# Kernel optimization log

Measured on AMD Instinct MI355X. Metric: run time of the kernel, lower is better.

The kernel has to match this reference:

```python
import jax, jax.numpy as jnp
import numpy as np

D_MODEL = 512
N_PAIRS = D_MODEL // 2
B, T = 8, 4096


def setup_inputs() -> dict:
    key = jax.random.key(0)
    ks = jax.random.split(key, 7)
    scale = 1.0 / np.sqrt(D_MODEL)
    return {
        "x_seq": jax.random.normal(ks[0], (B, T, D_MODEL), dtype=jnp.float32),
        "W_angle": jax.random.uniform(ks[1], (D_MODEL, N_PAIRS), jnp.float32, -scale, scale),
        "b_angle": jnp.zeros((N_PAIRS,), jnp.float32),
        "W_decay": jax.random.uniform(ks[2], (D_MODEL, 1), jnp.float32, -scale, scale),
        "b_decay": jnp.full((1,), 1.4, jnp.float32),
        "W_input": jax.random.uniform(ks[3], (D_MODEL, D_MODEL), jnp.float32, -scale, scale),
        "b_input": jax.random.uniform(ks[4], (D_MODEL,), jnp.float32, -scale, scale),
    }


def _givens_ssm(x_seq, W_angle, b_angle, W_decay, b_decay, W_input, b_input):
    Bb, Tt, D = x_seq.shape
    P = D // 2
    angles = jnp.einsum("btd,dp->btp", x_seq, W_angle) + b_angle          # [B,T,P]
    decays = jax.nn.sigmoid(jnp.einsum("btd,dk->btk", x_seq, W_decay) + b_decay)[..., 0]  # [B,T]
    inj = jnp.einsum("btd,de->bte", x_seq, W_input) + b_input              # [B,T,D]
    inj = inj.reshape(Bb, Tt, P, 2)

    # scan over time: h_t = decay_t * Rot(angles_t) h_{t-1} + inj_t, pairwise 2x2 rotations
    def step(h, inp):
        a, d, u = inp  # a:[B,P], d:[B], u:[B,P,2]
        c, s = jnp.cos(a), jnp.sin(a)
        he = c * h[..., 0] - s * h[..., 1]
        ho = s * h[..., 0] + c * h[..., 1]
        h_new = d[:, None, None] * jnp.stack([he, ho], axis=-1) + u
        return h_new, h_new

    h0 = jnp.zeros((Bb, P, 2), x_seq.dtype)
    xs = (jnp.swapaxes(angles, 0, 1), jnp.swapaxes(decays, 0, 1), jnp.swapaxes(inj, 0, 1))
    _, states = jax.lax.scan(step, h0, xs)  # [T,B,P,2]
    return jnp.swapaxes(states, 0, 1).reshape(Bb, Tt, D)


def reference(x_seq, W_angle, b_angle, W_decay, b_decay, W_input, b_input):
    return _givens_ssm(x_seq, W_angle, b_angle, W_decay, b_decay, W_input, b_input)
```

## Files before the change

### kernel.cpp

```cpp
#include <hip/hip_runtime.h>
#include <math.h>

typedef _Float16 half_t;
typedef __attribute__((ext_vector_type(8))) _Float16 half8;
typedef __attribute__((ext_vector_type(4))) _Float16 half4;
typedef __attribute__((ext_vector_type(2))) _Float16 half2v;
typedef __attribute__((ext_vector_type(4))) float floatx4;

#define BATCH   8
#define SEQ     4096
#define DM      512
#define NP      256
#define M_TOT   32768
#define NTOT    768
#define CHUNKS  256
#define CHUNK_LEN 16

__device__ __forceinline__ void async_load16(const void* g, void* l) {
    __builtin_amdgcn_global_load_lds((const __attribute__((address_space(1))) void*)g,
                                     (__attribute__((address_space(3))) void*)l,
                                     16, 0, 0);
}

__global__ __launch_bounds__(256) void decay_convert(const float* __restrict__ X,
                                                     const float* __restrict__ Wd,
                                                     const float* __restrict__ bd,
                                                     float* __restrict__ dec,
                                                     half_t* __restrict__ Xh) {
    const int wave = threadIdx.x >> 6;
    const int lane = threadIdx.x & 63;
    const int row0 = blockIdx.x * 8 + wave * 2;
    const float4* x0 = (const float4*)(X + (size_t)row0 * DM);
    const float4* x1 = x0 + 128;
    const float4* wd = (const float4*)Wd;
    float4 a0 = x0[2 * lane], a1 = x0[2 * lane + 1];
    float4 b0 = x1[2 * lane], b1 = x1[2 * lane + 1];
    float4 w0 = wd[2 * lane], w1 = wd[2 * lane + 1];
    float s0 = a0.x * w0.x + a0.y * w0.y + a0.z * w0.z + a0.w * w0.w
             + a1.x * w1.x + a1.y * w1.y + a1.z * w1.z + a1.w * w1.w;
    float s1 = b0.x * w0.x + b0.y * w0.y + b0.z * w0.z + b0.w * w0.w
             + b1.x * w1.x + b1.y * w1.y + b1.z * w1.z + b1.w * w1.w;
    half8 h0 = {(half_t)a0.x, (half_t)a0.y, (half_t)a0.z, (half_t)a0.w,
                (half_t)a1.x, (half_t)a1.y, (half_t)a1.z, (half_t)a1.w};
    half8 h1 = {(half_t)b0.x, (half_t)b0.y, (half_t)b0.z, (half_t)b0.w,
                (half_t)b1.x, (half_t)b1.y, (half_t)b1.z, (half_t)b1.w};
    *(half8*)(Xh + (size_t)row0 * DM + lane * 8) = h0;
    *(half8*)(Xh + (size_t)(row0 + 1) * DM + lane * 8) = h1;
#pragma unroll
    for (int off = 32; off > 0; off >>= 1) {
        s0 += __shfl_down(s0, off, 64);
        s1 += __shfl_down(s1, off, 64);
    }
    if (lane == 0) {
        dec[row0]     = 1.0f / (1.0f + __expf(-(s0 + bd[0])));
        dec[row0 + 1] = 1.0f / (1.0f + __expf(-(s1 + bd[0])));
    }
}

__global__ __launch_bounds__(256) void wcat_transpose(const float* __restrict__ Wi,
                                                      const float* __restrict__ Wa,
                                                      half_t* __restrict__ Wt) {
    const int idx = blockIdx.x * 256 + threadIdx.x;
    const int n = idx >> 9;
    const int k = idx & 511;
    float v = (n < DM) ? Wi[(size_t)k * DM + n] : Wa[(size_t)k * NP + (n - DM)];
    Wt[idx] = (half_t)v;
}

__global__ __launch_bounds__(256) void gemm_fused(const half_t* __restrict__ Xh,
                                                  const half_t* __restrict__ Wt,
                                                  const float* __restrict__ bi,
                                                  const float* __restrict__ ba,
                                                  half_t* __restrict__ inj,
                                                  half_t* __restrict__ angles) {
    __shared__ __align__(16) char As[8192];
    __shared__ __align__(16) char Bs[8192];

    const int bm   = blockIdx.x;
    const int bn   = blockIdx.y;
    const int tid  = threadIdx.x;
    const int wave = tid >> 6;
    const int lane = tid & 63;
    const int quad = lane >> 4;
    const int l16  = lane & 15;
    const int wrow = wave >> 1;
    const int wcol = wave & 1;

    floatx4 acc[4][4];
#pragma unroll
    for (int i = 0; i < 4; ++i)
#pragma unroll
        for (int j = 0; j < 4; ++j) acc[i][j] = (floatx4){0.f, 0.f, 0.f, 0.f};

    const int s0 = wave * 128 + lane;
    const int s1 = s0 + 64;
    const int r0 = s0 >> 2, kql0 = (s0 & 3) ^ ((r0 >> 1) & 3);
    const int r1 = s1 >> 2, kql1 = (s1 & 3) ^ ((r1 >> 1) & 3);
    const half_t* gA0 = Xh + (size_t)(bm * 128 + r0) * DM + kql0 * 8;
    const half_t* gA1 = Xh + (size_t)(bm * 128 + r1) * DM + kql1 * 8;
    const half_t* gB0 = Wt + (size_t)(bn * 128 + r0) * DM + kql0 * 8;
    const half_t* gB1 = Wt + (size_t)(bn * 128 + r1) * DM + kql1 * 8;
    char* lA0 = As + wave * 2048;
    char* lA1 = As + wave * 2048 + 1024;
    char* lB0 = Bs + wave * 2048;
    char* lB1 = Bs + wave * 2048 + 1024;

    for (int k0 = 0; k0 < DM; k0 += 32) {
        async_load16(gA0 + k0, lA0);
        async_load16(gA1 + k0, lA1);
        async_load16(gB0 + k0, lB0);
        async_load16(gB1 + k0, lB1);
        __syncthreads();

        half8 af[4], bf[4];
#pragma unroll
        for (int mt = 0; mt < 4; ++mt) {
            const int r = wrow * 64 + mt * 16 + l16;
            af[mt] = *(const half8*)(As + r * 64 + ((quad ^ ((r >> 1) & 3)) << 4));
        }
#pragma unroll
        for (int nt = 0; nt < 4; ++nt) {
            const int r = wcol * 64 + nt * 16 + l16;
            bf[nt] = *(const half8*)(Bs + r * 64 + ((quad ^ ((r >> 1) & 3)) << 4));
        }
#pragma unroll
        for (int mt = 0; mt < 4; ++mt)
#pragma unroll
            for (int nt = 0; nt < 4; ++nt)
                acc[mt][nt] = __builtin_amdgcn_mfma_f32_16x16x32_f16(af[mt], bf[nt],
                                                                     acc[mt][nt], 0, 0, 0);
        __syncthreads();
    }

    const int colbase = bn * 128 + wcol * 64;
#pragma unroll
    for (int nt = 0; nt < 4; ++nt) {
        const int col = colbase + nt * 16 + l16;
        const bool is_inj = col < DM;
        const float bias = is_inj ? bi[col] : ba[col - DM];
#pragma unroll
        for (int mt = 0; mt < 4; ++mt) {
            const int rowb = bm * 128 + wrow * 64 + mt * 16 + quad * 4;
#pragma unroll
            for (int r = 0; r < 4; ++r) {
                const float v = acc[mt][nt][r] + bias;
                const int row = rowb + r;
                if (is_inj) inj[(size_t)row * DM + col] = (half_t)v;
                else        angles[(size_t)row * NP + (col - DM)] = (half_t)v;
            }
        }
    }
}

__global__ __launch_bounds__(256) void scan_sum1(const half_t* __restrict__ angles,
                                                 const float* __restrict__ decays,
                                                 const half_t* __restrict__ inj,
                                                 float* __restrict__ thetaC,
                                                 float4* __restrict__ hend,
                                                 float* __restrict__ Dprod) {
    const int b   = blockIdx.x >> 7;
    const int sub = threadIdx.x >> 7;
    const int th  = threadIdx.x & 127;
    const int c   = (blockIdx.x & 127) * 2 + sub;
    const int p0  = th * 2;
    const int t0  = c * CHUNK_LEN;

    const half_t* ap = angles + (size_t)(b * SEQ + t0) * NP + p0;
    const half4*  up = (const half4*)(inj + (size_t)(b * SEQ + t0) * DM) + th;
    const float*  dp = decays + b * SEQ + t0;

    half2v ab[2][8]; half4 ub[2][8]; float db[2][8];
#pragma unroll
    for (int j = 0; j < 8; ++j) {
        ab[0][j] = *(const half2v*)(ap + (size_t)j * NP);
        ub[0][j] = up[(size_t)j * 128];
        db[0][j] = dp[j];
    }

    float h0a = 0, h1a = 0, h0b = 0, h1b = 0, tha = 0, thb = 0, dc = 1.0f;
#pragma unroll
    for (int g = 0; g < 2; ++g) {
        const int cur = g & 1, nxt = cur ^ 1;
        if (g < 1) {
#pragma unroll
            for (int j = 0; j < 8; ++j) {
                const int t = (g + 1) * 8 + j;
                ab[nxt][j] = *(const half2v*)(ap + (size_t)t * NP);
                ub[nxt][j] = up[(size_t)t * 128];
                db[nxt][j] = dp[t];
            }
        }
#pragma unroll
        for (int j = 0; j < 8; ++j) {
            float a0 = (float)ab[cur][j][0], a1 = (float)ab[cur][j][1];
            half4 uh = ub[cur][j];
            float d  = db[cur][j];
            float s0, c0, s1, c1;
            __sincosf(a0, &s0, &c0);
            __sincosf(a1, &s1, &c1);
            float n0a = fmaf(d, c0 * h0a - s0 * h1a, (float)uh[0]);
            float n1a = fmaf(d, s0 * h0a + c0 * h1a, (float)uh[1]);
            float n0b = fmaf(d, c1 * h0b - s1 * h1b, (float)uh[2]);
            float n1b = fmaf(d, s1 * h0b + c1 * h1b, (float)uh[3]);
            h0a = n0a; h1a = n1a; h0b = n0b; h1b = n1b;
            tha += a0; thb += a1; dc *= d;
        }
    }
    const size_t cbase = (size_t)(b * CHUNKS + c) * NP + p0;
    *(float2*)(thetaC + cbase) = make_float2(tha, thb);
    hend[cbase >> 1] = make_float4(h0a, h1a, h0b, h1b);
    if (th == 0) Dprod[b * CHUNKS + c] = dc;
}

__global__ __launch_bounds__(256) void scan_chunks(const float* __restrict__ thetaC,
                                                   const float4* __restrict__ hend,
                                                   const float* __restrict__ Dprod,
                                                   float4* __restrict__ hentry) {
    const int b  = blockIdx.x >> 7;
    const int pp = blockIdx.x & 127;
    const int c  = threadIdx.x;

    __shared__ float  sTa[256], sTb[256], sD[256];
    __shared__ float4 sV[256];

    const size_t idx = (size_t)(b * CHUNKS + c);
    const float2 th2 = *(const float2*)(thetaC + idx * NP + pp * 2);
    float4 v = hend[idx * 128 + pp];
    float  D = Dprod[idx];
    float tha = th2.x, thb = th2.y;

    sTa[c] = tha; sTb[c] = thb; sD[c] = D; sV[c] = v;

#pragma unroll
    for (int o = 1; o < 256; o <<= 1) {
        __syncthreads();
        float lta = 0.f, ltb = 0.f, lD = 0.f;
        float4 lv = make_float4(0.f, 0.f, 0.f, 0.f);
        const bool has = (c >= o);
        if (has) { lta = sTa[c - o]; ltb = sTb[c - o]; lD = sD[c - o]; lv = sV[c - o]; }
        __syncthreads();
        if (has) {
            float s0, c0, s1, c1;
            __sincosf(tha, &s0, &c0);
            __sincosf(thb, &s1, &c1);
            v.x = fmaf(D, c0 * lv.x - s0 * lv.y, v.x);
            v.y = fmaf(D, s0 * lv.x + c0 * lv.y, v.y);
            v.z = fmaf(D, c1 * lv.z - s1 * lv.w, v.z);
            v.w = fmaf(D, s1 * lv.z + c1 * lv.w, v.w);
            tha += lta; thb += ltb; D *= lD;
            sTa[c] = tha; sTb[c] = thb; sD[c] = D; sV[c] = v;
        }
    }
    __syncthreads();
    const float4 e = (c == 0) ? make_float4(0.f, 0.f, 0.f, 0.f) : sV[c - 1];
    hentry[idx * 128 + pp] = e;
}

__global__ __launch_bounds__(256) void scan_final(const half_t* __restrict__ angles,
                                                  const float* __restrict__ decays,
                                                  const half_t* __restrict__ inj,
                                                  const float4* __restrict__ hentry,
                                                  float* __restrict__ out) {
    const int b   = blockIdx.x >> 7;
    const int sub = threadIdx.x >> 7;
    const int th  = threadIdx.x & 127;
    const int c   = (blockIdx.x & 127) * 2 + sub;
    const int p0  = th * 2;
    const int t0  = c * CHUNK_LEN;

    const half_t* ap = angles + (size_t)(b * SEQ + t0) * NP + p0;
    const half4*  up = (const half4*)(inj + (size_t)(b * SEQ + t0) * DM) + th;
    float4*       op = (float4*)out + (size_t)(b * SEQ + t0) * 128 + (p0 >> 1);
    const float*  dp = decays + b * SEQ + t0;

    float4 v = hentry[(size_t)(b * CHUNKS + c) * 128 + (p0 >> 1)];
    float h0a = v.x, h1a = v.y, h0b = v.z, h1b = v.w;

    half2v ab[2][8]; half4 ub[2][8]; float db[2][8];
#pragma unroll
    for (int j = 0; j < 8; ++j) {
        ab[0][j] = *(const half2v*)(ap + (size_t)j * NP);
        ub[0][j] = up[(size_t)j * 128];
        db[0][j] = dp[j];
    }

#pragma unroll
    for (int g = 0; g < 2; ++g) {
        const int cur = g & 1, nxt = cur ^ 1;
        if (g < 1) {
#pragma unroll
            for (int j = 0; j < 8; ++j) {
                const int t = (g + 1) * 8 + j;
                ab[nxt][j] = *(const half2v*)(ap + (size_t)t * NP);
                ub[nxt][j] = up[(size_t)t * 128];
                db[nxt][j] = dp[t];
            }
        }
#pragma unroll
        for (int j = 0; j < 8; ++j) {
            const int t = g * 8 + j;
            float a0 = (float)ab[cur][j][0], a1 = (float)ab[cur][j][1];
            half4 uh = ub[cur][j];
            float d  = db[cur][j];
            float s0, c0, s1, c1;
            __sincosf(a0, &s0, &c0);
            __sincosf(a1, &s1, &c1);
            float n0a = fmaf(d, c0 * h0a - s0 * h1a, (float)uh[0]);
            float n1a = fmaf(d, s0 * h0a + c0 * h1a, (float)uh[1]);
            float n0b = fmaf(d, c1 * h0b - s1 * h1b, (float)uh[2]);
            float n1b = fmaf(d, s1 * h0b + c1 * h1b, (float)uh[3]);
            h0a = n0a; h1a = n1a; h0b = n0b; h1b = n1b;
            op[(size_t)t * 128] = make_float4(h0a, h1a, h0b, h1b);
        }
    }
}

extern "C" void kernel_launch(void* const* d_in, const int* in_sizes, int n_in,
                              void* d_out, int out_size, void* d_ws, size_t ws_size,
                              hipStream_t stream) {
    const float* x  = (const float*)d_in[0];
    const float* Wa = (const float*)d_in[1];
    const float* ba = (const float*)d_in[2];
    const float* Wd = (const float*)d_in[3];
    const float* bd = (const float*)d_in[4];
    const float* Wi = (const float*)d_in[5];
    const float* bi = (const float*)d_in[6];
    float* out = (float*)d_out;

    char* ws = (char*)d_ws;
    half_t* x_h     = (half_t*)(ws);
    float*  thetaC  = (float*)(ws);
    float4* hend    = (float4*)(ws + 2097152);
    float*  Dprod   = (float*)(ws + 6291456);
    float4* hentry  = (float4*)(ws + 6299648);
    half_t* inj_h   = (half_t*)(ws + 33554432);
    half_t* angles  = (half_t*)(ws + 67108864);
    float*  decays  = (float*)(ws + 83886080);
    half_t* Wcat_t  = (half_t*)(ws + 84017152);

    decay_convert<<<M_TOT / 8, 256, 0, stream>>>(x, Wd, bd, decays, x_h);
    wcat_transpose<<<(NTOT * DM) / 256, 256, 0, stream>>>(Wi, Wa, Wcat_t);
    gemm_fused<<<dim3(M_TOT / 128, NTOT / 128), 256, 0, stream>>>(x_h, Wcat_t, bi, ba, inj_h, angles);

    scan_sum1<<<BATCH * CHUNKS / 2, 256, 0, stream>>>(angles, decays, inj_h, thetaC, hend, Dprod);
    scan_chunks<<<BATCH * 128, 256, 0, stream>>>(thetaC, hend, Dprod, hentry);
    scan_final<<<BATCH * CHUNKS / 2, 256, 0, stream>>>(angles, decays, inj_h, hentry, out);
}
```

Measured before the change: 217.6 us.

## Stage GEMM epilogue through LDS for coalesced stores; fold weight transpose into convert

The GEMM epilogue now writes the biased fp16 results into shared memory in two 64-row halves, then writes them out as coalesced 16-byte vectors instead of scattered 2-byte stores. The separate weight-transpose kernel is removed and its work runs in 6 extra blocks of the decay/convert kernel, saving one launch. The catch is that those 6 blocks each loop serially over 256 elements per thread with strided reads, so they may finish after the rest of the kernel. The epilogue also adds extra barriers and LDS traffic.

```diff
diff --git a/kernel.cpp b/kernel.cpp
--- a/kernel.cpp
+++ b/kernel.cpp
@@ -26,7 +26,21 @@
                                                      const float* __restrict__ Wd,
                                                      const float* __restrict__ bd,
                                                      float* __restrict__ dec,
-                                                     half_t* __restrict__ Xh) {
+                                                     half_t* __restrict__ Xh,
+                                                     const float* __restrict__ Wi,
+                                                     const float* __restrict__ Wa,
+                                                     half_t* __restrict__ Wt) {
+    if (blockIdx.x >= M_TOT / 8) {
+        const int idx = (blockIdx.x - M_TOT / 8) * 65536 + threadIdx.x * 256;
+        for (int e = 0; e < 256; ++e) {
+            const int i = idx + e;
+            const int n = i >> 9;
+            const int k = i & 511;
+            float v = (n < DM) ? Wi[(size_t)k * DM + n] : Wa[(size_t)k * NP + (n - DM)];
+            Wt[i] = (half_t)v;
+        }
+        return;
+    }
     const int wave = threadIdx.x >> 6;
     const int lane = threadIdx.x & 63;
     const int row0 = blockIdx.x * 8 + wave * 2;
@@ -57,16 +71,6 @@
     }
 }
 
-__global__ __launch_bounds__(256) void wcat_transpose(const float* __restrict__ Wi,
-                                                      const float* __restrict__ Wa,
-                                                      half_t* __restrict__ Wt) {
-    const int idx = blockIdx.x * 256 + threadIdx.x;
-    const int n = idx >> 9;
-    const int k = idx & 511;
-    float v = (n < DM) ? Wi[(size_t)k * DM + n] : Wa[(size_t)k * NP + (n - DM)];
-    Wt[idx] = (half_t)v;
-}
-
 __global__ __launch_bounds__(256) void gemm_fused(const half_t* __restrict__ Xh,
                                                   const half_t* __restrict__ Wt,
                                                   const float* __restrict__ bi,
@@ -132,22 +136,43 @@
         __syncthreads();
     }
 
-    const int colbase = bn * 128 + wcol * 64;
+    const bool  is_inj = (bn < 4);
+    half_t*     dst    = is_inj ? inj    : angles;
+    const int   ldd    = is_inj ? DM     : NP;
+    const int   cb     = is_inj ? bn * 128 : bn * 128 - DM;
+
+    float bias[4];
 #pragma unroll
     for (int nt = 0; nt < 4; ++nt) {
-        const int col = colbase + nt * 16 + l16;
-        const bool is_inj = col < DM;
-        const float bias = is_inj ? bi[col] : ba[col - DM];
-#pragma unroll
-        for (int mt = 0; mt < 4; ++mt) {
-            const int rowb = bm * 128 + wrow * 64 + mt * 16 + quad * 4;
-#pragma unroll
-            for (int r = 0; r < 4; ++r) {
-                const float v = acc[mt][nt][r] + bias;
-                const int row = rowb + r;
-                if (is_inj) inj[(size_t)row * DM + col] = (half_t)v;
-                else        angles[(size_t)row * NP + (col - DM)] = (half_t)v;
-            }
+        const int colt = wcol * 64 + nt * 16 + l16;
+        bias[nt] = is_inj ? bi[bn * 128 + colt] : ba[bn * 128 + colt - DM];
+    }
+
+    half_t* Cs = (half_t*)As;
+#pragma unroll
+    for (int rh = 0; rh < 2; ++rh) {
+        __syncthreads();
+        if (wrow == rh) {
+#pragma unroll
+            for (int mt = 0; mt < 4; ++mt)
+#pragma unroll
+                for (int nt = 0; nt < 4; ++nt)
+#pragma unroll
+                    for (int r = 0; r < 4; ++r) {
+                        const int lr = mt * 16 + quad * 4 + r;
+                        const int lc = wcol * 64 + nt * 16 + l16;
+                        Cs[lr * 128 + lc] = (half_t)(acc[mt][nt][r] + bias[nt]);
+                    }
+        }
+        __syncthreads();
+#pragma unroll
+        for (int it = 0; it < 4; ++it) {
+            const int idx = it * 256 + tid;
+            const int rr  = idx >> 4;
+            const int cc  = (idx & 15) * 8;
+            const int grow = bm * 128 + rh * 64 + rr;
+            half8 v = *(half8*)(Cs + rr * 128 + cc);
+            *(half8*)(dst + (size_t)grow * ldd + cb + cc) = v;
         }
     }
 }
@@ -338,8 +363,7 @@
     float*  decays  = (float*)(ws + 83886080);
     half_t* Wcat_t  = (half_t*)(ws + 84017152);
 
-    decay_convert<<<M_TOT / 8, 256, 0, stream>>>(x, Wd, bd, decays, x_h);
-    wcat_transpose<<<(NTOT * DM) / 256, 256, 0, stream>>>(Wi, Wa, Wcat_t);
+    decay_convert<<<M_TOT / 8 + 6, 256, 0, stream>>>(x, Wd, bd, decays, x_h, Wi, Wa, Wcat_t);
     gemm_fused<<<dim3(M_TOT / 128, NTOT / 128), 256, 0, stream>>>(x_h, Wcat_t, bi, ba, inj_h, angles);
 
     scan_sum1<<<BATCH * CHUNKS / 2, 256, 0, stream>>>(angles, decays, inj_h, thetaC, hend, Dprod);
```

New measurement: 251.5 us. 1.16x slower.
